# Kernel tuning notes

Measured on AMD Instinct MI355X. Metric: run time of the kernel, lower is better.

The kernel has to match this reference:

```python
import jax, jax.numpy as jnp
import numpy as np

VOCAB, EMB, HID, NCLS = 50257, 48, 128, 2000
B, S = 512, 1024


def setup_inputs() -> dict:
    key = jax.random.key(0)
    ks = jax.random.split(key, 8)
    x = jax.random.randint(ks[0], (B, S), 0, VOCAB)
    emb_table = jax.random.normal(ks[1], (VOCAB, EMB), dtype=jnp.float32)
    emb_table = emb_table.at[0].set(0.0)  # padding_idx=0
    k_ih = 1.0 / np.sqrt(HID)
    w_ih = jax.random.uniform(ks[2], (4 * HID, EMB), minval=-k_ih, maxval=k_ih, dtype=jnp.float32)
    w_hh = jax.random.uniform(ks[3], (4 * HID, HID), minval=-k_ih, maxval=k_ih, dtype=jnp.float32)
    b_ih = jax.random.uniform(ks[4], (4 * HID,), minval=-k_ih, maxval=k_ih, dtype=jnp.float32)
    b_hh = jax.random.uniform(ks[5], (4 * HID,), minval=-k_ih, maxval=k_ih, dtype=jnp.float32)
    k_fc = 1.0 / np.sqrt(HID)
    w_fc = jax.random.uniform(ks[6], (NCLS, HID), minval=-k_fc, maxval=k_fc, dtype=jnp.float32)
    b_fc = jax.random.uniform(ks[7], (NCLS,), minval=-k_fc, maxval=k_fc, dtype=jnp.float32)
    return {"x": x, "emb_table": emb_table, "w_ih": w_ih, "w_hh": w_hh,
            "b_ih": b_ih, "b_hh": b_hh, "w_fc": w_fc, "b_fc": b_fc}


def _lstm_last_hidden(e, w_ih, w_hh, b_ih, b_hh):
    # e: [B, S, E]. Precompute input contributions for all timesteps (one big GEMM).
    xg = jnp.einsum('bse,ge->bsg', e, w_ih) + b_ih + b_hh  # [B, S, 4H]
    xg = jnp.transpose(xg, (1, 0, 2))                      # [S, B, 4H]
    Bn = e.shape[0]
    h0 = jnp.zeros((Bn, HID), e.dtype)
    c0 = jnp.zeros((Bn, HID), e.dtype)

    def step(carry, xg_t):
        h, c = carry
        g = xg_t + h @ w_hh.T                              # [B, 4H]
        i, f, gg, o = jnp.split(g, 4, axis=-1)             # PyTorch gate order i,f,g,o
        i = jax.nn.sigmoid(i)
        f = jax.nn.sigmoid(f)
        gg = jnp.tanh(gg)
        o = jax.nn.sigmoid(o)
        c = f * c + i * gg
        h = o * jnp.tanh(c)
        return (h, c), None

    (h_n, _), _ = jax.lax.scan(step, (h0, c0), xg)
    return h_n


def reference(x, emb_table, w_ih, w_hh, b_ih, b_hh, w_fc, b_fc):
    e = emb_table[x]                                       # [B, S, E] gather
    h_n = _lstm_last_hidden(e, w_ih, w_hh, b_ih, b_hh)     # [B, H]
    return h_n @ w_fc.T + b_fc                             # [B, NCLS]
```

## Files before the change

### kernel.cpp

```cpp
#include <hip/hip_runtime.h>

#define DI __device__ __forceinline__

typedef unsigned int uint;
typedef unsigned short ushort;
typedef _Float16 half2t __attribute__((ext_vector_type(2)));

#define VOCAB 50257
#define NEMB 48
#define HID 128
#define G4 512
#define NCLS 2000
#define BATCH 512
#define SEQ 1024

#if __has_builtin(__builtin_amdgcn_fdot2)
DI float fdot2(half2t a, half2t b, float c) { return __builtin_amdgcn_fdot2(a, b, c, false); }
#else
DI float fdot2(half2t a, half2t b, float c) { return c + (float)a.x * (float)b.x + (float)a.y * (float)b.y; }
#endif

DI float sigm(float x) {
  return __builtin_amdgcn_rcpf(1.0f + __builtin_amdgcn_exp2f(-1.4426950408889634f * x));
}
DI float tanhfast(float x) {
  return 1.0f - 2.0f * __builtin_amdgcn_rcpf(__builtin_amdgcn_exp2f(2.8853900817779268f * x) + 1.0f);
}

#define VROWS 32
__global__ __launch_bounds__(512) void build_P(
    const float* __restrict__ emb, const float* __restrict__ w_ih,
    const float* __restrict__ b_ih, const float* __restrict__ b_hh,
    _Float16* __restrict__ P)
{
  __shared__ __align__(16) float eL[VROWS][NEMB];
  const int tid = threadIdx.x;
  const int v0 = blockIdx.x * VROWS;
  int nrows = VOCAB - v0; if (nrows > VROWS) nrows = VROWS;

  for (int f = tid; f < nrows * NEMB; f += 512)
    eL[f / NEMB][f % NEMB] = emb[(size_t)v0 * NEMB + f];

  float w[NEMB];
  {
    const float* wr = w_ih + (size_t)tid * NEMB;
#pragma unroll
    for (int k = 0; k < NEMB; k++) w[k] = wr[k];
  }
  float bias = b_ih[tid] + b_hh[tid];
  __syncthreads();

  for (int v = 0; v < nrows; v++) {
    const float4* e4 = (const float4*)&eL[v][0];
    float a = bias;
#pragma unroll
    for (int k = 0; k < NEMB / 4; k++) {
      float4 e = e4[k];
      a += w[4 * k] * e.x + w[4 * k + 1] * e.y + w[4 * k + 2] * e.z + w[4 * k + 3] * e.w;
    }
    P[(size_t)(v0 + v) * G4 + tid] = (_Float16)a;
  }
}

template<bool USE_P>
__global__ __launch_bounds__(256, 2) void lstm_scan(
    const int* __restrict__ x, const float* __restrict__ emb,
    const float* __restrict__ w_ih, const float* __restrict__ w_hh,
    const float* __restrict__ b_ih, const float* __restrict__ b_hh,
    const _Float16* __restrict__ P, float* __restrict__ hout)
{
  __shared__ int tokL[SEQ];
  __shared__ __align__(16) _Float16 h16[HID];
  __shared__ float g32[G4];
  __shared__ __align__(8) half2t e16[2][NEMB / 2];

  const int tid = threadIdx.x;
  const int b = blockIdx.x;

  {
    const int* xp = x + (size_t)b * SEQ;
#pragma unroll
    for (int i = 0; i < SEQ / 256; i++) tokL[tid + 256 * i] = xp[tid + 256 * i];
  }

  half2t w0[HID / 2], w1[HID / 2];
  {
    const float4* wr0 = (const float4*)(w_hh + (size_t)tid * HID);
    const float4* wr1 = (const float4*)(w_hh + (size_t)(tid + 256) * HID);
#pragma unroll
    for (int k = 0; k < HID / 4; k++) {
      float4 a = wr0[k];
      half2t p; p.x = (_Float16)a.x; p.y = (_Float16)a.y; w0[2 * k] = p;
      p.x = (_Float16)a.z; p.y = (_Float16)a.w; w0[2 * k + 1] = p;
      float4 bv = wr1[k];
      p.x = (_Float16)bv.x; p.y = (_Float16)bv.y; w1[2 * k] = p;
      p.x = (_Float16)bv.z; p.y = (_Float16)bv.w; w1[2 * k + 1] = p;
    }
  }
  half2t wih0[NEMB / 2], wih1[NEMB / 2];
  float bias0 = 0.0f, bias1 = 0.0f;
  if (!USE_P) {
    const float* wr0 = w_ih + (size_t)tid * NEMB;
    const float* wr1 = w_ih + (size_t)(tid + 256) * NEMB;
#pragma unroll
    for (int k = 0; k < NEMB / 2; k++) {
      half2t p;
      p.x = (_Float16)wr0[2 * k]; p.y = (_Float16)wr0[2 * k + 1]; wih0[k] = p;
      p.x = (_Float16)wr1[2 * k]; p.y = (_Float16)wr1[2 * k + 1]; wih1[k] = p;
    }
    bias0 = b_ih[tid] + b_hh[tid];
    bias1 = b_ih[tid + 256] + b_hh[tid + 256];
  }
  if (tid < HID) h16[tid] = (_Float16)0.0f;
  __syncthreads();

  float c = 0.0f;
  _Float16 pa0{}, pa1{}, pb0{}, pb1{};
  float2 einfl = {0.0f, 0.0f};
  if (USE_P) {
    const _Float16* r0 = P + (size_t)tokL[0] * G4;
    const _Float16* r1 = P + (size_t)tokL[1] * G4;
    pa0 = r0[tid]; pa1 = r0[tid + 256];
    pb0 = r1[tid]; pb1 = r1[tid + 256];
  } else {
    if (tid < NEMB / 2) {
      float2 e0 = ((const float2*)(emb + (size_t)tokL[0] * NEMB))[tid];
      einfl    = ((const float2*)(emb + (size_t)tokL[1] * NEMB))[tid];
      half2t p; p.x = (_Float16)e0.x; p.y = (_Float16)e0.y;
      e16[0][tid] = p;
    }
  }
  __syncthreads();

#define STEP(t, par) do {                                                      \
    int tc = (t) + 2; if (tc > SEQ - 1) tc = SEQ - 1;                          \
    float xg0, xg1;                                                            \
    if (USE_P) {                                                               \
      xg0 = (float)((par) ? pb0 : pa0);                                        \
      xg1 = (float)((par) ? pb1 : pa1);                                        \
      const _Float16* rn = P + (size_t)tokL[tc] * G4;        \
      _Float16 n0 = rn[tid], n1 = rn[tid + 256];                               \
      if ((par) == 0) { pa0 = n0; pa1 = n1; } else { pb0 = n0; pb1 = n1; }     \
    } else {                                                                   \
      if (tid < NEMB / 2) {                                                    \
        half2t p; p.x = (_Float16)einfl.x; p.y = (_Float16)einfl.y;            \
        e16[((t) + 1) & 1][tid] = p;                                           \
        einfl = ((const float2*)(emb + (size_t)tokL[tc] * NEMB))[tid];         \
      }                                                                        \
      xg0 = bias0; xg1 = bias1;                                                \
      _Pragma("unroll")                                                        \
      for (int k = 0; k < NEMB / 2; k++) {                                     \
        xg0 = fdot2(wih0[k], e16[(par)][k], xg0);                              \
        xg1 = fdot2(wih1[k], e16[(par)][k], xg1);                              \
      }                                                                        \
    }                                                                          \
    const uint4* hv = (const uint4*)h16;                                       \
    float s0 = xg0, u0 = 0.0f, s1 = xg1, u1 = 0.0f;                            \
    _Pragma("unroll")                                                          \
    for (int kt = 0; kt < HID / 8; kt++) {                                     \
      uint4 hq = hv[kt];                                                       \
      half2t ha = __builtin_bit_cast(half2t, hq.x);                            \
      half2t hb = __builtin_bit_cast(half2t, hq.y);                            \
      half2t hc = __builtin_bit_cast(half2t, hq.z);                            \
      half2t hd = __builtin_bit_cast(half2t, hq.w);                            \
      s0 = fdot2(w0[4 * kt + 0], ha, s0);                                      \
      u0 = fdot2(w0[4 * kt + 1], hb, u0);                                      \
      s0 = fdot2(w0[4 * kt + 2], hc, s0);                                      \
      u0 = fdot2(w0[4 * kt + 3], hd, u0);                                      \
      s1 = fdot2(w1[4 * kt + 0], ha, s1);                                      \
      u1 = fdot2(w1[4 * kt + 1], hb, u1);                                      \
      s1 = fdot2(w1[4 * kt + 2], hc, s1);                                      \
      u1 = fdot2(w1[4 * kt + 3], hd, u1);                                      \
    }                                                                          \
    g32[tid] = s0 + u0;                                                        \
    g32[tid + 256] = s1 + u1;                                                  \
    __syncthreads();                                                           \
    if (tid < HID) {                                                           \
      float gi = g32[tid],           gf = g32[HID + tid];                      \
      float gc = g32[2 * HID + tid], go = g32[3 * HID + tid];                  \
      float fi = sigm(gi), ff = sigm(gf), gt = tanhfast(gc), fo = sigm(go);    \
      c = ff * c + fi * gt;                                                    \
      float hh = fo * tanhfast(c);                                             \
      h16[tid] = (_Float16)hh;                                                 \
      if ((t) == SEQ - 1) hout[(size_t)b * HID + tid] = hh;                    \
    }                                                                          \
    __syncthreads();                                                           \
  } while (0)

  for (int t = 0; t < SEQ; t += 2) { STEP(t, 0); STEP(t + 1, 1); }
#undef STEP
}

#define FCR 64
#define FCC 64
__global__ __launch_bounds__(256) void fc_kernel(
    const float* __restrict__ h, const float* __restrict__ w_fc,
    const float* __restrict__ b_fc, float* __restrict__ out)
{
  __shared__ float aT[HID][FCR];
  __shared__ float bT[HID][FCC];
  const int tid = threadIdx.x;
  const int r0 = blockIdx.y * FCR;
  const int c0 = blockIdx.x * FCC;

  for (int f = tid; f < FCR * (HID / 4); f += 256) {
    int row = f >> 5, q = f & 31;
    float4 v = ((const float4*)h)[(((size_t)(r0 + row)) << 5) + q];
    aT[4 * q + 0][row] = v.x; aT[4 * q + 1][row] = v.y;
    aT[4 * q + 2][row] = v.z; aT[4 * q + 3][row] = v.w;
    int wrow = c0 + row;
    float4 wv;
    if (wrow < NCLS) wv = ((const float4*)w_fc)[(((size_t)wrow) << 5) + q];
    else { wv.x = 0.f; wv.y = 0.f; wv.z = 0.f; wv.w = 0.f; }
    bT[4 * q + 0][row] = wv.x; bT[4 * q + 1][row] = wv.y;
    bT[4 * q + 2][row] = wv.z; bT[4 * q + 3][row] = wv.w;
  }
  __syncthreads();

  const int cr = tid & 15, rr = tid >> 4;
  float acc[4][4];
#pragma unroll
  for (int i = 0; i < 4; i++)
#pragma unroll
    for (int j = 0; j < 4; j++) acc[i][j] = 0.0f;

#pragma unroll 4
  for (int k = 0; k < HID; k++) {
    float4 av = *(const float4*)&aT[k][4 * rr];
    float4 bv = *(const float4*)&bT[k][4 * cr];
    float a[4] = {av.x, av.y, av.z, av.w};
    float bb[4] = {bv.x, bv.y, bv.z, bv.w};
#pragma unroll
    for (int i = 0; i < 4; i++)
#pragma unroll
      for (int j = 0; j < 4; j++) acc[i][j] += a[i] * bb[j];
  }

#pragma unroll
  for (int j = 0; j < 4; j++) {
    int cc = c0 + 4 * cr + j;
    if (cc < NCLS) {
      float bias = b_fc[cc];
#pragma unroll
      for (int i = 0; i < 4; i++)
        out[(size_t)(r0 + 4 * rr + i) * NCLS + cc] = acc[i][j] + bias;
    }
  }
}

extern "C" void kernel_launch(void* const* d_in, const int* in_sizes, int n_in,
                              void* d_out, int out_size, void* d_ws, size_t ws_size,
                              hipStream_t stream) {
  const int*   xx   = (const int*)d_in[0];
  const float* emb  = (const float*)d_in[1];
  const float* w_ih = (const float*)d_in[2];
  const float* w_hh = (const float*)d_in[3];
  const float* b_ih = (const float*)d_in[4];
  const float* b_hh = (const float*)d_in[5];
  const float* w_fc = (const float*)d_in[6];
  const float* b_fc = (const float*)d_in[7];
  float* out = (float*)d_out;

  const size_t pbytes = (size_t)VOCAB * G4 * sizeof(_Float16);
  const size_t palign = (pbytes + 255) & ~(size_t)255;
  const size_t hbytes = (size_t)BATCH * HID * sizeof(float);

  float* hout;
  if (ws_size >= palign + hbytes) {
    _Float16* P = (_Float16*)d_ws;
    hout = (float*)((char*)d_ws + palign);
    build_P<<<(VOCAB + VROWS - 1) / VROWS, 512, 0, stream>>>(emb, w_ih, b_ih, b_hh, P);
    lstm_scan<true><<<BATCH, 256, 0, stream>>>(xx, emb, w_ih, w_hh, b_ih, b_hh, P, hout);
  } else {
    hout = (float*)d_ws;
    lstm_scan<false><<<BATCH, 256, 0, stream>>>(xx, emb, w_ih, w_hh, b_ih, b_hh,
                                                (const _Float16*)nullptr, hout);
  }
  dim3 fcg((NCLS + FCC - 1) / FCC, BATCH / FCR);
  fc_kernel<<<fcg, 256, 0, stream>>>(hout, w_fc, b_fc, out);
}
```

Before: 1.005 ms.

## Split LSTM recurrent dot products across two thread halves with shared partial-sum reduction

Doubles the scan block to 512 threads. Each half computes partial gate dot products over half of the hidden dimension, so each thread holds only half the recurrent weights. Partial sums go to shared memory as float2 and are added before the activations. This shortens the per-step serial dot-product chain and frees registers for more wavefronts, at the cost of more threads sharing each barrier and an extra add per gate.

```diff
diff --git a/kernel.cpp b/kernel.cpp
--- a/kernel.cpp
+++ b/kernel.cpp
@@ -63,7 +63,7 @@
 }
 
 template<bool USE_P>
-__global__ __launch_bounds__(256, 2) void lstm_scan(
+__global__ __launch_bounds__(512, 4) void lstm_scan(
     const int* __restrict__ x, const float* __restrict__ emb,
     const float* __restrict__ w_ih, const float* __restrict__ w_hh,
     const float* __restrict__ b_ih, const float* __restrict__ b_hh,
@@ -71,24 +71,27 @@
 {
   __shared__ int tokL[SEQ];
   __shared__ __align__(16) _Float16 h16[HID];
-  __shared__ float g32[G4];
+  __shared__ __align__(8) float2 g2[G4];
   __shared__ __align__(8) half2t e16[2][NEMB / 2];
 
   const int tid = threadIdx.x;
   const int b = blockIdx.x;
+  const int col = tid & 255;
+  const int kh = tid >> 8;
+  const int koff = kh * (HID / 2);
 
   {
     const int* xp = x + (size_t)b * SEQ;
 #pragma unroll
-    for (int i = 0; i < SEQ / 256; i++) tokL[tid + 256 * i] = xp[tid + 256 * i];
-  }
-
-  half2t w0[HID / 2], w1[HID / 2];
+    for (int i = 0; i < SEQ / 512; i++) tokL[tid + 512 * i] = xp[tid + 512 * i];
+  }
+
+  half2t w0[HID / 4], w1[HID / 4];
   {
-    const float4* wr0 = (const float4*)(w_hh + (size_t)tid * HID);
-    const float4* wr1 = (const float4*)(w_hh + (size_t)(tid + 256) * HID);
-#pragma unroll
-    for (int k = 0; k < HID / 4; k++) {
+    const float4* wr0 = (const float4*)(w_hh + (size_t)col * HID + koff);
+    const float4* wr1 = (const float4*)(w_hh + (size_t)(col + 256) * HID + koff);
+#pragma unroll
+    for (int k = 0; k < HID / 8; k++) {
       float4 a = wr0[k];
       half2t p; p.x = (_Float16)a.x; p.y = (_Float16)a.y; w0[2 * k] = p;
       p.x = (_Float16)a.z; p.y = (_Float16)a.w; w0[2 * k + 1] = p;
@@ -99,17 +102,17 @@
   }
   half2t wih0[NEMB / 2], wih1[NEMB / 2];
   float bias0 = 0.0f, bias1 = 0.0f;
-  if (!USE_P) {
-    const float* wr0 = w_ih + (size_t)tid * NEMB;
-    const float* wr1 = w_ih + (size_t)(tid + 256) * NEMB;
+  if (!USE_P && kh == 0) {
+    const float* wr0 = w_ih + (size_t)col * NEMB;
+    const float* wr1 = w_ih + (size_t)(col + 256) * NEMB;
 #pragma unroll
     for (int k = 0; k < NEMB / 2; k++) {
       half2t p;
       p.x = (_Float16)wr0[2 * k]; p.y = (_Float16)wr0[2 * k + 1]; wih0[k] = p;
       p.x = (_Float16)wr1[2 * k]; p.y = (_Float16)wr1[2 * k + 1]; wih1[k] = p;
     }
-    bias0 = b_ih[tid] + b_hh[tid];
-    bias1 = b_ih[tid + 256] + b_hh[tid + 256];
+    bias0 = b_ih[col] + b_hh[col];
+    bias1 = b_ih[col + 256] + b_hh[col + 256];
   }
   if (tid < HID) h16[tid] = (_Float16)0.0f;
   __syncthreads();
@@ -118,10 +121,12 @@
   _Float16 pa0{}, pa1{}, pb0{}, pb1{};
   float2 einfl = {0.0f, 0.0f};
   if (USE_P) {
-    const _Float16* r0 = P + (size_t)tokL[0] * G4;
-    const _Float16* r1 = P + (size_t)tokL[1] * G4;
-    pa0 = r0[tid]; pa1 = r0[tid + 256];
-    pb0 = r1[tid]; pb1 = r1[tid + 256];
+    if (kh == 0) {
+      const _Float16* r0 = P + (size_t)tokL[0] * G4;
+      const _Float16* r1 = P + (size_t)tokL[1] * G4;
+      pa0 = r0[col]; pa1 = r0[col + 256];
+      pb0 = r1[col]; pb1 = r1[col + 256];
+    }
   } else {
     if (tid < NEMB / 2) {
       float2 e0 = ((const float2*)(emb + (size_t)tokL[0] * NEMB))[tid];
@@ -133,31 +138,36 @@
   __syncthreads();
 
 #define STEP(t, par) do {                                                      \
-    int tc = (t) + 2; if (tc > SEQ - 1) tc = SEQ - 1;                          \
     float xg0, xg1;                                                            \
     if (USE_P) {                                                               \
-      xg0 = (float)((par) ? pb0 : pa0);                                        \
-      xg1 = (float)((par) ? pb1 : pa1);                                        \
-      const _Float16* rn = P + (size_t)tokL[tc] * G4;        \
-      _Float16 n0 = rn[tid], n1 = rn[tid + 256];                               \
-      if ((par) == 0) { pa0 = n0; pa1 = n1; } else { pb0 = n0; pb1 = n1; }     \
+      if (kh == 0) {                                                           \
+        int tc = (t) + 2; if (tc > SEQ - 1) tc = SEQ - 1;                      \
+        xg0 = (float)((par) ? pb0 : pa0);                                      \
+        xg1 = (float)((par) ? pb1 : pa1);                                      \
+        const _Float16* rn = P + (size_t)tokL[tc] * G4;      \
+        _Float16 n0 = rn[col], n1 = rn[col + 256];                             \
+        if ((par) == 0) { pa0 = n0; pa1 = n1; } else { pb0 = n0; pb1 = n1; }   \
+      } else { xg0 = 0.0f; xg1 = 0.0f; }                                       \
     } else {                                                                   \
       if (tid < NEMB / 2) {                                                    \
+        int tc = (t) + 2; if (tc > SEQ - 1) tc = SEQ - 1;                      \
         half2t p; p.x = (_Float16)einfl.x; p.y = (_Float16)einfl.y;            \
         e16[((t) + 1) & 1][tid] = p;                                           \
         einfl = ((const float2*)(emb + (size_t)tokL[tc] * NEMB))[tid];         \
       }                                                                        \
-      xg0 = bias0; xg1 = bias1;                                                \
-      _Pragma("unroll")                                                        \
-      for (int k = 0; k < NEMB / 2; k++) {                                     \
-        xg0 = fdot2(wih0[k], e16[(par)][k], xg0);                              \
-        xg1 = fdot2(wih1[k], e16[(par)][k], xg1);                              \
-      }                                                                        \
+      if (kh == 0) {                                                           \
+        xg0 = bias0; xg1 = bias1;                                              \
+        _Pragma("unroll")                                                      \
+        for (int k = 0; k < NEMB / 2; k++) {                                   \
+          xg0 = fdot2(wih0[k], e16[(par)][k], xg0);                            \
+          xg1 = fdot2(wih1[k], e16[(par)][k], xg1);                            \
+        }                                                                      \
+      } else { xg0 = 0.0f; xg1 = 0.0f; }                                       \
     }                                                                          \
-    const uint4* hv = (const uint4*)h16;                                       \
+    const uint4* hv = (const uint4*)h16 + (kh << 3);                           \
     float s0 = xg0, u0 = 0.0f, s1 = xg1, u1 = 0.0f;                            \
     _Pragma("unroll")                                                          \
-    for (int kt = 0; kt < HID / 8; kt++) {                                     \
+    for (int kt = 0; kt < HID / 16; kt++) {                                    \
       uint4 hq = hv[kt];                                                       \
       half2t ha = __builtin_bit_cast(half2t, hq.x);                            \
       half2t hb = __builtin_bit_cast(half2t, hq.y);                            \
@@ -172,12 +182,14 @@
       s1 = fdot2(w1[4 * kt + 2], hc, s1);                                      \
       u1 = fdot2(w1[4 * kt + 3], hd, u1);                                      \
     }                                                                          \
-    g32[tid] = s0 + u0;                                                        \
-    g32[tid + 256] = s1 + u1;                                                  \
+    ((float*)&g2[col])[kh] = s0 + u0;                                          \
+    ((float*)&g2[col + 256])[kh] = s1 + u1;                                    \
     __syncthreads();                                                           \
     if (tid < HID) {                                                           \
-      float gi = g32[tid],           gf = g32[HID + tid];                      \
-      float gc = g32[2 * HID + tid], go = g32[3 * HID + tid];                  \
+      float2 v0 = g2[tid],           v1 = g2[HID + tid];                       \
+      float2 v2 = g2[2 * HID + tid], v3 = g2[3 * HID + tid];                   \
+      float gi = v0.x + v0.y, gf = v1.x + v1.y;                                \
+      float gc = v2.x + v2.y, go = v3.x + v3.y;                                \
       float fi = sigm(gi), ff = sigm(gf), gt = tanhfast(gc), fo = sigm(go);    \
       c = ff * c + fi * gt;                                                    \
       float hh = fo * tanhfast(c);                                             \
@@ -270,10 +282,10 @@
     _Float16* P = (_Float16*)d_ws;
     hout = (float*)((char*)d_ws + palign);
     build_P<<<(VOCAB + VROWS - 1) / VROWS, 512, 0, stream>>>(emb, w_ih, b_ih, b_hh, P);
-    lstm_scan<true><<<BATCH, 256, 0, stream>>>(xx, emb, w_ih, w_hh, b_ih, b_hh, P, hout);
+    lstm_scan<true><<<BATCH, 512, 0, stream>>>(xx, emb, w_ih, w_hh, b_ih, b_hh, P, hout);
   } else {
     hout = (float*)d_ws;
-    lstm_scan<false><<<BATCH, 256, 0, stream>>>(xx, emb, w_ih, w_hh, b_ih, b_hh,
+    lstm_scan<false><<<BATCH, 512, 0, stream>>>(xx, emb, w_ih, w_hh, b_ih, b_hh,
                                                 (const _Float16*)nullptr, hout);
   }
   dim3 fcg((NCLS + FCC - 1) / FCC, BATCH / FCR);
```

New measurement: 1.012 ms. No clear change (+0.7%).
